# Optimization experiments

Hardware: AMD Instinct MI355X
Metric: run time of the kernel (lower is better)

The kernel has to match this reference:

```python
import jax, jax.numpy as jnp
import numpy as np

K = 20
EPS = 1e-5
SLOPE = 0.2


def _leaky(v):
    return jnp.where(v >= 0, v, SLOPE * v)


def _instnorm(v, axes):
    # InstanceNorm with affine=False: normalize per (batch, channel) over spatial axes,
    # biased variance, eps=1e-5 (torch default).
    mean = jnp.mean(v, axis=axes, keepdims=True)
    var = jnp.mean((v - mean) ** 2, axis=axes, keepdims=True)
    return (v - mean) * jax.lax.rsqrt(var + EPS)


def _knn_idx(x, k):
    # x: [B, C, N]; returns indices of k nearest neighbors (self included), [B, N, k]
    inner = -2.0 * jnp.einsum('bcn,bcm->bnm', x, x)
    xx = jnp.sum(x * x, axis=1)                      # [B, N]
    pd = -xx[:, :, None] - inner - xx[:, None, :]    # negative squared distance
    return jax.lax.top_k(pd, k)[1]


def _edge_conv(x, w):
    # x: [B, C, N]; w: [O, 2C]. Returns [B, O, N] after max-pool over k neighbors.
    B, C, N = x.shape
    idx = _knn_idx(x, K)                              # [B, N, K]
    xt = jnp.transpose(x, (0, 2, 1))                  # [B, N, C]
    b_idx = jnp.arange(B)[:, None, None]
    nb = xt[b_idx, idx]                               # [B, N, K, C] gathered neighbors
    ctr = xt[:, :, None, :]                           # [B, N, 1, C]
    feat = jnp.concatenate([nb - ctr, jnp.broadcast_to(ctr, nb.shape)], axis=-1)
    h = jnp.einsum('oc,bnkc->bonk', w, feat)          # 1x1 conv as GEMM -> [B, O, N, K]
    h = _leaky(_instnorm(h, (2, 3)))
    return jnp.max(h, axis=-1)                        # [B, O, N]


def setup_inputs() -> dict:
    key = jax.random.key(0)
    ks = jax.random.split(key, 6)
    B, N, feat_dim = 8, 2048, 512
    return {
        'x': jax.random.normal(ks[0], (B, N, 3), dtype=jnp.float32),
        'w1': jax.random.normal(ks[1], (64, 6), dtype=jnp.float32) * 0.1,
        'w2': jax.random.normal(ks[2], (64, 128), dtype=jnp.float32) * 0.1,
        'w3': jax.random.normal(ks[3], (128, 128), dtype=jnp.float32) * 0.1,
        'w4': jax.random.normal(ks[4], (256, 256), dtype=jnp.float32) * 0.1,
        'w5': jax.random.normal(ks[5], (feat_dim, 512), dtype=jnp.float32) * 0.1,
    }


def reference(x, w1, w2, w3, w4, w5):
    xc = jnp.transpose(x, (0, 2, 1))                  # [B, 3, N]
    x1 = _edge_conv(xc, w1)                           # [B, 64, N]
    x2 = _edge_conv(x1, w2)                           # [B, 64, N]
    x3 = _edge_conv(x2, w3)                           # [B, 128, N]
    x4 = _edge_conv(x3, w4)                           # [B, 256, N]
    cat = jnp.concatenate([x1, x2, x3, x4], axis=1)   # [B, 512, N]
    h = jnp.einsum('oc,bcn->bon', w5, cat)            # conv5 (1x1 conv1d)
    feat = _leaky(_instnorm(h, (2,)))
    return feat                                       # [B, feat_dim, N]
```

## Files before the change

kernel.cpp:

```cpp
#include <hip/hip_runtime.h>
#include <math.h>

#define NPTS 2048
#define NB 8
#define KNN 20
#define EPSI 1e-5f
#define SLOPE 0.2f
#define CHUNK 512

typedef short bf16x8 __attribute__((ext_vector_type(8)));
typedef float f32x4 __attribute__((ext_vector_type(4)));

__device__ __forceinline__ unsigned short f2bf(float x) {
    union { float f; unsigned u; } v; v.f = x;
    unsigned r = v.u + 0x7FFF + ((v.u >> 16) & 1u);
    return (unsigned short)(r >> 16);
}
__device__ __forceinline__ float bf2f(unsigned short h) {
    union { unsigned u; float f; } v; v.u = ((unsigned)h) << 16; return v.f;
}

__global__ __launch_bounds__(256) void transpose_kernel(const float* __restrict__ xin,
                                                        float* __restrict__ xc) {
    int g = blockIdx.x * 256 + threadIdx.x;
    int b = g / NPTS, n = g % NPTS;
    float v0 = xin[(size_t)g * 3 + 0];
    float v1 = xin[(size_t)g * 3 + 1];
    float v2 = xin[(size_t)g * 3 + 2];
    xc[((size_t)b * 3 + 0) * NPTS + n] = v0;
    xc[((size_t)b * 3 + 1) * NPTS + n] = v1;
    xc[((size_t)b * 3 + 2) * NPTS + n] = v2;
}

__global__ __launch_bounds__(256) void xx_kernel(const float* __restrict__ x, int bstride, int C,
                                                 float* __restrict__ xx) {
    int g = blockIdx.x * 256 + threadIdx.x;
    int b = g / NPTS, n = g % NPTS;
    const float* p = x + (size_t)b * bstride + n;
    float s = 0.f;
    for (int c = 0; c < C; ++c) { float v = p[(size_t)c * NPTS]; s += v * v; }
    xx[g] = s;
}

__global__ __launch_bounds__(256) void pd_gemm2(const float* __restrict__ x, int bstride, int C,
                                                const float* __restrict__ xx,
                                                float* __restrict__ pd, int r0) {
    __shared__ float As[16][128];
    __shared__ float Bs[16][128];
    int b = blockIdx.z;
    int nbase_l = blockIdx.y * 128;
    int mbase = blockIdx.x * 128;
    int tx = threadIdx.x & 15, ty = threadIdx.x >> 4;
    int tid = threadIdx.x;
    float acc[8][8] = {};
    const float* xb = x + (size_t)b * bstride;

    for (int c0 = 0; c0 < C; c0 += 16) {
        int KC = min(16, C - c0);
        for (int t = tid; t < 512; t += 256) {
            int cc = t >> 5, j4 = (t & 31) * 4;
            float4 av = make_float4(0.f, 0.f, 0.f, 0.f), bv = av;
            if (cc < KC) {
                av = *(const float4*)&xb[(size_t)(c0 + cc) * NPTS + r0 + nbase_l + j4];
                bv = *(const float4*)&xb[(size_t)(c0 + cc) * NPTS + mbase + j4];
            }
            *(float4*)&As[cc][j4] = av;
            *(float4*)&Bs[cc][j4] = bv;
        }
        __syncthreads();
        #pragma unroll
        for (int cc = 0; cc < 16; ++cc) {
            float av[8], bv[8];
            *(float4*)&av[0] = *(float4*)&As[cc][ty * 8];
            *(float4*)&av[4] = *(float4*)&As[cc][ty * 8 + 4];
            *(float4*)&bv[0] = *(float4*)&Bs[cc][tx * 8];
            *(float4*)&bv[4] = *(float4*)&Bs[cc][tx * 8 + 4];
            #pragma unroll
            for (int i = 0; i < 8; ++i)
                #pragma unroll
                for (int j = 0; j < 8; ++j)
                    acc[i][j] += av[i] * bv[j];
        }
        __syncthreads();
    }

    const float* xxb = xx + (size_t)b * NPTS;
    #pragma unroll
    for (int i = 0; i < 8; ++i) {
        int nl = nbase_l + ty * 8 + i;
        float xn = xxb[r0 + nl];
        float4 o0, o1;
        o0.x = 2.f * acc[i][0] - xn - xxb[mbase + tx*8 + 0];
        o0.y = 2.f * acc[i][1] - xn - xxb[mbase + tx*8 + 1];
        o0.z = 2.f * acc[i][2] - xn - xxb[mbase + tx*8 + 2];
        o0.w = 2.f * acc[i][3] - xn - xxb[mbase + tx*8 + 3];
        o1.x = 2.f * acc[i][4] - xn - xxb[mbase + tx*8 + 4];
        o1.y = 2.f * acc[i][5] - xn - xxb[mbase + tx*8 + 5];
        o1.z = 2.f * acc[i][6] - xn - xxb[mbase + tx*8 + 6];
        o1.w = 2.f * acc[i][7] - xn - xxb[mbase + tx*8 + 7];
        *(float4*)&pd[((size_t)b * CHUNK + nl) * NPTS + mbase + tx*8] = o0;
        *(float4*)&pd[((size_t)b * CHUNK + nl) * NPTS + mbase + tx*8 + 4] = o1;
    }
}

__global__ __launch_bounds__(256) void topk_kernel(const float* __restrict__ pd,
                                                   int* __restrict__ idxout, int r0) {
    int wid = (blockIdx.x * 256 + threadIdx.x) >> 6;
    int lane = threadIdx.x & 63;
    int b = wid / CHUNK;
    int nl = wid % CHUNK;
    int n = r0 + nl;
    const float* row = pd + ((size_t)b * CHUNK + nl) * NPTS;

    float v[32];
    #pragma unroll
    for (int j = 0; j < 32; ++j) v[j] = row[lane + 64 * j];

    unsigned mask = 0u;
    int saved = 0;
    for (int t = 0; t < KNN; ++t) {
        float best = -INFINITY; int bj = 0;
        #pragma unroll
        for (int j = 0; j < 32; ++j) {
            bool ok = ((mask >> j) & 1u) == 0u;
            if (ok && v[j] > best) { best = v[j]; bj = j; }
        }
        int midx = lane + 64 * bj;
        #pragma unroll
        for (int off = 32; off > 0; off >>= 1) {
            float ov = __shfl_xor(best, off);
            int om = __shfl_xor(midx, off);
            if (ov > best || (ov == best && om < midx)) { best = ov; midx = om; }
        }
        if (lane == t) saved = midx;
        if ((midx & 63) == lane) mask |= 1u << (midx >> 6);
    }
    if (lane < KNN) idxout[((size_t)b * NPTS + n) * KNN + lane] = saved;
}

__global__ __launch_bounds__(256) void yz_gemm(const float* __restrict__ x, int bstride, int C, int O,
                                               const float* __restrict__ w,
                                               float* __restrict__ y, float* __restrict__ z) {
    __shared__ float Xs[128 * 64];
    __shared__ float Ws[4 * 256];
    int b = blockIdx.z;
    int mbase = blockIdx.x * 64;
    int obase = blockIdx.y * 4;
    int tx = threadIdx.x & 63, ty = threadIdx.x >> 6;
    int tid = threadIdx.x;
    const float* xb = x + (size_t)b * bstride;

    for (int t = tid; t < C * 64; t += 256) {
        int cc = t >> 6, j = t & 63;
        Xs[cc * 64 + j] = xb[(size_t)cc * NPTS + mbase + j];
    }
    int C2 = 2 * C;
    for (int t = tid; t < 4 * C2; t += 256) {
        int ol = t / C2, c = t % C2;
        Ws[ol * C2 + c] = w[(size_t)(obase + ol) * C2 + c];
    }
    __syncthreads();

    int o = obase + ty;
    const float* wr = &Ws[ty * C2];
    float ya = 0.f, za = 0.f;
    for (int c = 0; c < C; ++c) {
        float v = Xs[c * 64 + tx];
        float wd = wr[c], wc = wr[C + c];
        ya += wd * v;
        za += (wc - wd) * v;
    }
    y[((size_t)b * O + o) * NPTS + mbase + tx] = ya;
    z[((size_t)b * O + o) * NPTS + mbase + tx] = za;
}

__global__ __launch_bounds__(256) void gather_norm(const float* __restrict__ y,
                                                   const float* __restrict__ z,
                                                   const int* __restrict__ idx,
                                                   float* __restrict__ cat, int coff, int O) {
    __shared__ float yrow[NPTS];
    __shared__ float red[8];
    int o = blockIdx.x, b = blockIdx.y;
    int tid = threadIdx.x;
    const float* yr = y + ((size_t)b * O + o) * NPTS;
    for (int i = tid; i < NPTS / 4; i += 256)
        ((float4*)yrow)[i] = ((const float4*)yr)[i];
    __syncthreads();

    const float* zr = z + ((size_t)b * O + o) * NPTS;
    float s1 = 0.f, s2 = 0.f;
    float hm[8];
    #pragma unroll
    for (int r = 0; r < 8; ++r) {
        int n = r * 256 + tid;
        float zv = zr[n];
        const int* ip = idx + ((size_t)b * NPTS + n) * KNN;
        float mx = -INFINITY;
        #pragma unroll
        for (int k = 0; k < KNN; ++k) {
            float h = yrow[ip[k]] + zv;
            s1 += h; s2 += h * h;
            mx = fmaxf(mx, h);
        }
        hm[r] = mx;
    }
    #pragma unroll
    for (int off = 32; off > 0; off >>= 1) {
        s1 += __shfl_xor(s1, off);
        s2 += __shfl_xor(s2, off);
    }
    int wv = tid >> 6, lane = tid & 63;
    if (lane == 0) { red[wv] = s1; red[4 + wv] = s2; }
    __syncthreads();
    float S1 = red[0] + red[1] + red[2] + red[3];
    float S2 = red[4] + red[5] + red[6] + red[7];
    const float inv = 1.f / (float)(NPTS * KNN);
    float mean = S1 * inv;
    float var = S2 * inv - mean * mean;
    float rs = 1.f / sqrtf(var + EPSI);
    float* dst = cat + ((size_t)b * 512 + coff + o) * NPTS;
    #pragma unroll
    for (int r = 0; r < 8; ++r) {
        float vv = (hm[r] - mean) * rs;
        dst[r * 256 + tid] = vv >= 0.f ? vv : SLOPE * vv;
    }
}

__global__ __launch_bounds__(256) void w5_prep(const float* __restrict__ w5,
                                               unsigned short* __restrict__ wh,
                                               unsigned short* __restrict__ wl) {
    int i = blockIdx.x * 256 + threadIdx.x;
    float x = w5[i];
    unsigned short h = f2bf(x);
    wh[i] = h;
    wl[i] = f2bf(x - bf2f(h));
}

__global__ __launch_bounds__(256) void catT_prep(const float* __restrict__ cat,
                                                 unsigned short* __restrict__ cth,
                                                 unsigned short* __restrict__ ctl) {
    __shared__ float t[32][33];
    int b = blockIdx.z;
    int n0 = blockIdx.x * 32, c0 = blockIdx.y * 32;
    int tx = threadIdx.x & 31, ty = threadIdx.x >> 5;
    #pragma unroll
    for (int r = 0; r < 4; ++r) {
        int ci = ty + r * 8;
        t[ci][tx] = cat[((size_t)b * 512 + c0 + ci) * NPTS + n0 + tx];
    }
    __syncthreads();
    #pragma unroll
    for (int r = 0; r < 4; ++r) {
        int ni = ty + r * 8;
        float x = t[tx][ni];
        unsigned short h = f2bf(x);
        size_t off = ((size_t)b * NPTS + n0 + ni) * 512 + c0 + tx;
        cth[off] = h;
        ctl[off] = f2bf(x - bf2f(h));
    }
}

__global__ __launch_bounds__(256) void final_gemm_mfma(const unsigned short* __restrict__ wh,
                                                       const unsigned short* __restrict__ wl,
                                                       const unsigned short* __restrict__ cth,
                                                       const unsigned short* __restrict__ ctl,
                                                       float* __restrict__ h) {
    int b = blockIdx.z;
    int nbase = blockIdx.x * 64, obase = blockIdx.y * 64;
    int w = threadIdx.x >> 6, l = threadIdx.x & 63;
    int wr = (w >> 1) * 32, wc = (w & 1) * 32;
    int lr = l & 15, lk = (l >> 4) * 8;

    f32x4 acc[2][2] = {};
    const unsigned short* aH = wh + (size_t)(obase + wr + lr) * 512 + lk;
    const unsigned short* aL = wl + (size_t)(obase + wr + lr) * 512 + lk;
    const unsigned short* bH = cth + ((size_t)b * NPTS + nbase + wc + lr) * 512 + lk;
    const unsigned short* bL = ctl + ((size_t)b * NPTS + nbase + wc + lr) * 512 + lk;

    for (int k0 = 0; k0 < 512; k0 += 32) {
        bf16x8 ah[2], al[2], bh[2], bl[2];
        #pragma unroll
        for (int mi = 0; mi < 2; ++mi) {
            ah[mi] = *(const bf16x8*)(aH + (size_t)mi * 16 * 512 + k0);
            al[mi] = *(const bf16x8*)(aL + (size_t)mi * 16 * 512 + k0);
        }
        #pragma unroll
        for (int ni = 0; ni < 2; ++ni) {
            bh[ni] = *(const bf16x8*)(bH + (size_t)ni * 16 * 512 + k0);
            bl[ni] = *(const bf16x8*)(bL + (size_t)ni * 16 * 512 + k0);
        }
        #pragma unroll
        for (int mi = 0; mi < 2; ++mi)
            #pragma unroll
            for (int ni = 0; ni < 2; ++ni) {
                acc[mi][ni] = __builtin_amdgcn_mfma_f32_16x16x32_bf16(ah[mi], bh[ni], acc[mi][ni], 0, 0, 0);
                acc[mi][ni] = __builtin_amdgcn_mfma_f32_16x16x32_bf16(ah[mi], bl[ni], acc[mi][ni], 0, 0, 0);
                acc[mi][ni] = __builtin_amdgcn_mfma_f32_16x16x32_bf16(al[mi], bh[ni], acc[mi][ni], 0, 0, 0);
            }
    }

    int orow = obase + wr + (l >> 4) * 4;
    int ncol = nbase + wc + lr;
    #pragma unroll
    for (int mi = 0; mi < 2; ++mi)
        #pragma unroll
        for (int r = 0; r < 4; ++r)
            #pragma unroll
            for (int ni = 0; ni < 2; ++ni)
                h[((size_t)b * 512 + orow + mi * 16 + r) * NPTS + ncol + ni * 16] = acc[mi][ni][r];
}

__global__ __launch_bounds__(256) void final_norm(const float* __restrict__ h,
                                                  float* __restrict__ out) {
    __shared__ float red[8];
    int o = blockIdx.x, b = blockIdx.y;
    int tid = threadIdx.x;
    const float* hr = h + ((size_t)b * 512 + o) * NPTS;
    float s1 = 0.f, s2 = 0.f;
    float v[8];
    #pragma unroll
    for (int r = 0; r < 8; ++r) {
        v[r] = hr[r * 256 + tid];
        s1 += v[r]; s2 += v[r] * v[r];
    }
    #pragma unroll
    for (int off = 32; off > 0; off >>= 1) {
        s1 += __shfl_xor(s1, off);
        s2 += __shfl_xor(s2, off);
    }
    int wv = tid >> 6, lane = tid & 63;
    if (lane == 0) { red[wv] = s1; red[4 + wv] = s2; }
    __syncthreads();
    float S1 = red[0] + red[1] + red[2] + red[3];
    float S2 = red[4] + red[5] + red[6] + red[7];
    const float inv = 1.f / (float)NPTS;
    float mean = S1 * inv;
    float var = S2 * inv - mean * mean;
    float rs = 1.f / sqrtf(var + EPSI);
    float* dst = out + ((size_t)b * 512 + o) * NPTS;
    #pragma unroll
    for (int r = 0; r < 8; ++r) {
        float vv = (v[r] - mean) * rs;
        dst[r * 256 + tid] = vv >= 0.f ? vv : SLOPE * vv;
    }
}

extern "C" void kernel_launch(void* const* d_in, const int* in_sizes, int n_in,
                              void* d_out, int out_size, void* d_ws, size_t ws_size,
                              hipStream_t stream) {
    const float* x_in = (const float*)d_in[0];
    const float* w1 = (const float*)d_in[1];
    const float* w2 = (const float*)d_in[2];
    const float* w3 = (const float*)d_in[3];
    const float* w4 = (const float*)d_in[4];
    const float* w5 = (const float*)d_in[5];
    float* out = (float*)d_out;
    float* ws = (float*)d_ws;

    float* region = ws;
    float* yb = region;
    float* zb = region + 4194304;
    float* pdb = region;
    int* idxb = (int*)(ws + 8388608);
    float* xxb = ws + 8388608 + 327680;
    float* xcb = xxb + NB * NPTS;
    float* cat = xcb + NB * 3 * NPTS;
    unsigned short* w5h = (unsigned short*)(cat + 8388608);
    unsigned short* w5l = w5h + 262144;
    unsigned short* cth = (unsigned short*)region;
    unsigned short* ctl = cth + (size_t)NB * NPTS * 512;
    float* hb = cat;

    transpose_kernel<<<NB * NPTS / 256, 256, 0, stream>>>(x_in, xcb);
    w5_prep<<<512 * 512 / 256, 256, 0, stream>>>(w5, w5h, w5l);

    const float* srcs[4] = {xcb, cat, cat + (size_t)64 * NPTS, cat + (size_t)128 * NPTS};
    int bstr[4] = {3 * NPTS, 512 * NPTS, 512 * NPTS, 512 * NPTS};
    int Cin[4] = {3, 64, 64, 128};
    int Oc[4] = {64, 64, 128, 256};
    const float* wl[4] = {w1, w2, w3, w4};
    int coffs[4] = {0, 64, 128, 256};

    for (int li = 0; li < 4; ++li) {
        xx_kernel<<<NB * NPTS / 256, 256, 0, stream>>>(srcs[li], bstr[li], Cin[li], xxb);
        for (int r0 = 0; r0 < NPTS; r0 += CHUNK) {
            pd_gemm2<<<dim3(NPTS / 128, CHUNK / 128, NB), 256, 0, stream>>>(
                srcs[li], bstr[li], Cin[li], xxb, pdb, r0);
            topk_kernel<<<NB * CHUNK / 4, 256, 0, stream>>>(pdb, idxb, r0);
        }
        yz_gemm<<<dim3(NPTS / 64, Oc[li] / 4, NB), dim3(256), 0, stream>>>(
            srcs[li], bstr[li], Cin[li], Oc[li], wl[li], yb, zb);
        gather_norm<<<dim3(Oc[li], NB), 256, 0, stream>>>(yb, zb, idxb, cat, coffs[li], Oc[li]);
    }

    catT_prep<<<dim3(NPTS / 32, 512 / 32, NB), 256, 0, stream>>>(cat, cth, ctl);
    final_gemm_mfma<<<dim3(NPTS / 64, 512 / 64, NB), 256, 0, stream>>>(w5h, w5l, cth, ctl, hb);
    final_norm<<<dim3(512, NB), 256, 0, stream>>>(hb, out);
}
```

Before: 1.530 ms.

## Double-buffer pd and final GEMMs, register-tile yz GEMM, batch channels in gather

The pairwise-distance GEMM now double-buffers its shared-memory tiles, so each iteration needs one barrier instead of two, and the final MFMA GEMM prefetches the next K-slice into registers. The yz GEMM is rewritten as a 64x64 register-tiled GEMM with K chunks staged in shared memory, replacing the one-output-per-thread dot product. gather_norm now handles four output channels per block, so each neighbour index load feeds four channels through a single float4 LDS read. The trade-off is higher register and LDS use, which may lower occupancy, and fewer blocks in the gather for small channel counts.

```diff
diff --git a/kernel.cpp b/kernel.cpp
--- a/kernel.cpp
+++ b/kernel.cpp
@@ -45,8 +45,8 @@
 __global__ __launch_bounds__(256) void pd_gemm2(const float* __restrict__ x, int bstride, int C,
                                                 const float* __restrict__ xx,
                                                 float* __restrict__ pd, int r0) {
-    __shared__ float As[16][128];
-    __shared__ float Bs[16][128];
+    __shared__ float As[2][16][128];
+    __shared__ float Bs[2][16][128];
     int b = blockIdx.z;
     int nbase_l = blockIdx.y * 128;
     int mbase = blockIdx.x * 128;
@@ -55,33 +55,68 @@
     float acc[8][8] = {};
     const float* xb = x + (size_t)b * bstride;
 
-    for (int c0 = 0; c0 < C; c0 += 16) {
-        int KC = min(16, C - c0);
+    {
+        int KC = min(16, C);
         for (int t = tid; t < 512; t += 256) {
             int cc = t >> 5, j4 = (t & 31) * 4;
             float4 av = make_float4(0.f, 0.f, 0.f, 0.f), bv = av;
             if (cc < KC) {
-                av = *(const float4*)&xb[(size_t)(c0 + cc) * NPTS + r0 + nbase_l + j4];
-                bv = *(const float4*)&xb[(size_t)(c0 + cc) * NPTS + mbase + j4];
-            }
-            *(float4*)&As[cc][j4] = av;
-            *(float4*)&Bs[cc][j4] = bv;
+                av = *(const float4*)&xb[(size_t)cc * NPTS + r0 + nbase_l + j4];
+                bv = *(const float4*)&xb[(size_t)cc * NPTS + mbase + j4];
+            }
+            *(float4*)&As[0][cc][j4] = av;
+            *(float4*)&Bs[0][cc][j4] = bv;
+        }
+    }
+    __syncthreads();
+
+    int cur = 0;
+    for (int c0 = 0; c0 < C; c0 += 16) {
+        int c1 = c0 + 16;
+        if (c1 < C) {
+            int KC = min(16, C - c1);
+            for (int t = tid; t < 512; t += 256) {
+                int cc = t >> 5, j4 = (t & 31) * 4;
+                float4 av = make_float4(0.f, 0.f, 0.f, 0.f), bv = av;
+                if (cc < KC) {
+                    av = *(const float4*)&xb[(size_t)(c1 + cc) * NPTS + r0 + nbase_l + j4];
+                    bv = *(const float4*)&xb[(size_t)(c1 + cc) * NPTS + mbase + j4];
+                }
+                *(float4*)&As[cur ^ 1][cc][j4] = av;
+                *(float4*)&Bs[cur ^ 1][cc][j4] = bv;
+            }
+        }
+        int KC = min(16, C - c0);
+        if (KC == 16) {
+            #pragma unroll
+            for (int cc = 0; cc < 16; ++cc) {
+                float av[8], bv[8];
+                *(float4*)&av[0] = *(float4*)&As[cur][cc][ty * 8];
+                *(float4*)&av[4] = *(float4*)&As[cur][cc][ty * 8 + 4];
+                *(float4*)&bv[0] = *(float4*)&Bs[cur][cc][tx * 8];
+                *(float4*)&bv[4] = *(float4*)&Bs[cur][cc][tx * 8 + 4];
+                #pragma unroll
+                for (int i = 0; i < 8; ++i)
+                    #pragma unroll
+                    for (int j = 0; j < 8; ++j)
+                        acc[i][j] += av[i] * bv[j];
+            }
+        } else {
+            for (int cc = 0; cc < KC; ++cc) {
+                float av[8], bv[8];
+                *(float4*)&av[0] = *(float4*)&As[cur][cc][ty * 8];
+                *(float4*)&av[4] = *(float4*)&As[cur][cc][ty * 8 + 4];
+                *(float4*)&bv[0] = *(float4*)&Bs[cur][cc][tx * 8];
+                *(float4*)&bv[4] = *(float4*)&Bs[cur][cc][tx * 8 + 4];
+                #pragma unroll
+                for (int i = 0; i < 8; ++i)
+                    #pragma unroll
+                    for (int j = 0; j < 8; ++j)
+                        acc[i][j] += av[i] * bv[j];
+            }
         }
         __syncthreads();
-        #pragma unroll
-        for (int cc = 0; cc < 16; ++cc) {
-            float av[8], bv[8];
-            *(float4*)&av[0] = *(float4*)&As[cc][ty * 8];
-            *(float4*)&av[4] = *(float4*)&As[cc][ty * 8 + 4];
-            *(float4*)&bv[0] = *(float4*)&Bs[cc][tx * 8];
-            *(float4*)&bv[4] = *(float4*)&Bs[cc][tx * 8 + 4];
-            #pragma unroll
-            for (int i = 0; i < 8; ++i)
-                #pragma unroll
-                for (int j = 0; j < 8; ++j)
-                    acc[i][j] += av[i] * bv[j];
-        }
-        __syncthreads();
+        cur ^= 1;
     }
 
     const float* xxb = xx + (size_t)b * NPTS;
@@ -138,91 +173,131 @@
     if (lane < KNN) idxout[((size_t)b * NPTS + n) * KNN + lane] = saved;
 }
 
-__global__ __launch_bounds__(256) void yz_gemm(const float* __restrict__ x, int bstride, int C, int O,
-                                               const float* __restrict__ w,
-                                               float* __restrict__ y, float* __restrict__ z) {
-    __shared__ float Xs[128 * 64];
-    __shared__ float Ws[4 * 256];
+__global__ __launch_bounds__(256) void yz_gemm2(const float* __restrict__ x, int bstride, int C, int O,
+                                                const float* __restrict__ w,
+                                                float* __restrict__ y, float* __restrict__ z) {
+    __shared__ float Xs[32][64];
+    __shared__ float Wd[32][64];
+    __shared__ float Wz[32][64];
     int b = blockIdx.z;
     int mbase = blockIdx.x * 64;
-    int obase = blockIdx.y * 4;
-    int tx = threadIdx.x & 63, ty = threadIdx.x >> 6;
+    int obase = blockIdx.y * 64;
     int tid = threadIdx.x;
+    int nq = tid & 15, oq = tid >> 4;
     const float* xb = x + (size_t)b * bstride;
-
-    for (int t = tid; t < C * 64; t += 256) {
-        int cc = t >> 6, j = t & 63;
-        Xs[cc * 64 + j] = xb[(size_t)cc * NPTS + mbase + j];
-    }
     int C2 = 2 * C;
-    for (int t = tid; t < 4 * C2; t += 256) {
-        int ol = t / C2, c = t % C2;
-        Ws[ol * C2 + c] = w[(size_t)(obase + ol) * C2 + c];
+    float accy[4][4] = {}, accz[4][4] = {};
+
+    for (int c0 = 0; c0 < C; c0 += 32) {
+        int KC = min(32, C - c0);
+        for (int t = tid; t < 512; t += 256) {
+            int cc = t >> 4, j4 = (t & 15) * 4;
+            float4 v = make_float4(0.f, 0.f, 0.f, 0.f);
+            if (cc < KC) v = *(const float4*)&xb[(size_t)(c0 + cc) * NPTS + mbase + j4];
+            *(float4*)&Xs[cc][j4] = v;
+        }
+        for (int t = tid; t < 2048; t += 256) {
+            int o = t >> 5, cc = t & 31;
+            float wd = 0.f, wz = 0.f;
+            if (cc < KC) {
+                wd = w[(size_t)(obase + o) * C2 + c0 + cc];
+                wz = w[(size_t)(obase + o) * C2 + C + c0 + cc] - wd;
+            }
+            Wd[cc][o] = wd; Wz[cc][o] = wz;
+        }
+        __syncthreads();
+        for (int cc = 0; cc < KC; ++cc) {
+            float xv[4], wdv[4], wzv[4];
+            *(float4*)xv  = *(float4*)&Xs[cc][nq * 4];
+            *(float4*)wdv = *(float4*)&Wd[cc][oq * 4];
+            *(float4*)wzv = *(float4*)&Wz[cc][oq * 4];
+            #pragma unroll
+            for (int i = 0; i < 4; ++i)
+                #pragma unroll
+                for (int j = 0; j < 4; ++j) {
+                    accy[i][j] += wdv[i] * xv[j];
+                    accz[i][j] += wzv[i] * xv[j];
+                }
+        }
+        __syncthreads();
+    }
+
+    #pragma unroll
+    for (int i = 0; i < 4; ++i) {
+        size_t off = ((size_t)b * O + obase + oq * 4 + i) * NPTS + mbase + nq * 4;
+        *(float4*)&y[off] = make_float4(accy[i][0], accy[i][1], accy[i][2], accy[i][3]);
+        *(float4*)&z[off] = make_float4(accz[i][0], accz[i][1], accz[i][2], accz[i][3]);
+    }
+}
+
+__global__ __launch_bounds__(256) void gather_norm2(const float* __restrict__ y,
+                                                    const float* __restrict__ z,
+                                                    const int* __restrict__ idx,
+                                                    float* __restrict__ cat, int coff, int O) {
+    __shared__ float yt[NPTS][4];
+    __shared__ float red[32];
+    int og = blockIdx.x * 4, b = blockIdx.y;
+    int tid = threadIdx.x;
+
+    for (int n = tid; n < NPTS; n += 256) {
+        float4 v;
+        v.x = y[((size_t)b * O + og + 0) * NPTS + n];
+        v.y = y[((size_t)b * O + og + 1) * NPTS + n];
+        v.z = y[((size_t)b * O + og + 2) * NPTS + n];
+        v.w = y[((size_t)b * O + og + 3) * NPTS + n];
+        *(float4*)&yt[n][0] = v;
     }
     __syncthreads();
 
-    int o = obase + ty;
-    const float* wr = &Ws[ty * C2];
-    float ya = 0.f, za = 0.f;
-    for (int c = 0; c < C; ++c) {
-        float v = Xs[c * 64 + tx];
-        float wd = wr[c], wc = wr[C + c];
-        ya += wd * v;
-        za += (wc - wd) * v;
-    }
-    y[((size_t)b * O + o) * NPTS + mbase + tx] = ya;
-    z[((size_t)b * O + o) * NPTS + mbase + tx] = za;
-}
-
-__global__ __launch_bounds__(256) void gather_norm(const float* __restrict__ y,
-                                                   const float* __restrict__ z,
-                                                   const int* __restrict__ idx,
-                                                   float* __restrict__ cat, int coff, int O) {
-    __shared__ float yrow[NPTS];
-    __shared__ float red[8];
-    int o = blockIdx.x, b = blockIdx.y;
-    int tid = threadIdx.x;
-    const float* yr = y + ((size_t)b * O + o) * NPTS;
-    for (int i = tid; i < NPTS / 4; i += 256)
-        ((float4*)yrow)[i] = ((const float4*)yr)[i];
-    __syncthreads();
-
-    const float* zr = z + ((size_t)b * O + o) * NPTS;
-    float s1 = 0.f, s2 = 0.f;
-    float hm[8];
-    #pragma unroll
+    float s1[4] = {0.f, 0.f, 0.f, 0.f}, s2[4] = {0.f, 0.f, 0.f, 0.f};
+    float hm[4][8];
     for (int r = 0; r < 8; ++r) {
         int n = r * 256 + tid;
-        float zv = zr[n];
         const int* ip = idx + ((size_t)b * NPTS + n) * KNN;
-        float mx = -INFINITY;
+        float zv[4], mx[4];
+        #pragma unroll
+        for (int j = 0; j < 4; ++j) {
+            zv[j] = z[((size_t)b * O + og + j) * NPTS + n];
+            mx[j] = -INFINITY;
+        }
         #pragma unroll
         for (int k = 0; k < KNN; ++k) {
-            float h = yrow[ip[k]] + zv;
-            s1 += h; s2 += h * h;
-            mx = fmaxf(mx, h);
-        }
-        hm[r] = mx;
-    }
-    #pragma unroll
-    for (int off = 32; off > 0; off >>= 1) {
-        s1 += __shfl_xor(s1, off);
-        s2 += __shfl_xor(s2, off);
-    }
+            int id = ip[k];
+            float4 yv = *(float4*)&yt[id][0];
+            float h0 = yv.x + zv[0]; s1[0] += h0; s2[0] += h0 * h0; mx[0] = fmaxf(mx[0], h0);
+            float h1 = yv.y + zv[1]; s1[1] += h1; s2[1] += h1 * h1; mx[1] = fmaxf(mx[1], h1);
+            float h2 = yv.z + zv[2]; s1[2] += h2; s2[2] += h2 * h2; mx[2] = fmaxf(mx[2], h2);
+            float h3 = yv.w + zv[3]; s1[3] += h3; s2[3] += h3 * h3; mx[3] = fmaxf(mx[3], h3);
+        }
+        #pragma unroll
+        for (int j = 0; j < 4; ++j) hm[j][r] = mx[j];
+    }
+    #pragma unroll
+    for (int off = 32; off > 0; off >>= 1)
+        #pragma unroll
+        for (int j = 0; j < 4; ++j) {
+            s1[j] += __shfl_xor(s1[j], off);
+            s2[j] += __shfl_xor(s2[j], off);
+        }
     int wv = tid >> 6, lane = tid & 63;
-    if (lane == 0) { red[wv] = s1; red[4 + wv] = s2; }
+    if (lane == 0)
+        #pragma unroll
+        for (int j = 0; j < 4; ++j) { red[j * 8 + wv] = s1[j]; red[j * 8 + 4 + wv] = s2[j]; }
     __syncthreads();
-    float S1 = red[0] + red[1] + red[2] + red[3];
-    float S2 = red[4] + red[5] + red[6] + red[7];
     const float inv = 1.f / (float)(NPTS * KNN);
-    float mean = S1 * inv;
-    float var = S2 * inv - mean * mean;
-    float rs = 1.f / sqrtf(var + EPSI);
-    float* dst = cat + ((size_t)b * 512 + coff + o) * NPTS;
-    #pragma unroll
-    for (int r = 0; r < 8; ++r) {
-        float vv = (hm[r] - mean) * rs;
-        dst[r * 256 + tid] = vv >= 0.f ? vv : SLOPE * vv;
+    #pragma unroll
+    for (int j = 0; j < 4; ++j) {
+        float S1 = red[j * 8 + 0] + red[j * 8 + 1] + red[j * 8 + 2] + red[j * 8 + 3];
+        float S2 = red[j * 8 + 4] + red[j * 8 + 5] + red[j * 8 + 6] + red[j * 8 + 7];
+        float mean = S1 * inv;
+        float var = S2 * inv - mean * mean;
+        float rs = 1.f / sqrtf(var + EPSI);
+        float* dst = cat + ((size_t)b * 512 + coff + og + j) * NPTS;
+        #pragma unroll
+        for (int r = 0; r < 8; ++r) {
+            float vv = (hm[j][r] - mean) * rs;
+            dst[r * 256 + tid] = vv >= 0.f ? vv : SLOPE * vv;
+        }
     }
 }
 
@@ -277,26 +352,36 @@
     const unsigned short* bH = cth + ((size_t)b * NPTS + nbase + wc + lr) * 512 + lk;
     const unsigned short* bL = ctl + ((size_t)b * NPTS + nbase + wc + lr) * 512 + lk;
 
+    bf16x8 ah[2][2], al[2][2], bh[2][2], bl[2][2];
+    #pragma unroll
+    for (int mi = 0; mi < 2; ++mi) {
+        ah[0][mi] = *(const bf16x8*)(aH + (size_t)mi * 16 * 512);
+        al[0][mi] = *(const bf16x8*)(aL + (size_t)mi * 16 * 512);
+        bh[0][mi] = *(const bf16x8*)(bH + (size_t)mi * 16 * 512);
+        bl[0][mi] = *(const bf16x8*)(bL + (size_t)mi * 16 * 512);
+    }
+
+    int buf = 0;
     for (int k0 = 0; k0 < 512; k0 += 32) {
-        bf16x8 ah[2], al[2], bh[2], bl[2];
-        #pragma unroll
-        for (int mi = 0; mi < 2; ++mi) {
-            ah[mi] = *(const bf16x8*)(aH + (size_t)mi * 16 * 512 + k0);
-            al[mi] = *(const bf16x8*)(aL + (size_t)mi * 16 * 512 + k0);
-        }
-        #pragma unroll
-        for (int ni = 0; ni < 2; ++ni) {
-            bh[ni] = *(const bf16x8*)(bH + (size_t)ni * 16 * 512 + k0);
-            bl[ni] = *(const bf16x8*)(bL + (size_t)ni * 16 * 512 + k0);
+        int nxt = buf ^ 1;
+        if (k0 + 32 < 512) {
+            #pragma unroll
+            for (int mi = 0; mi < 2; ++mi) {
+                ah[nxt][mi] = *(const bf16x8*)(aH + (size_t)mi * 16 * 512 + k0 + 32);
+                al[nxt][mi] = *(const bf16x8*)(aL + (size_t)mi * 16 * 512 + k0 + 32);
+                bh[nxt][mi] = *(const bf16x8*)(bH + (size_t)mi * 16 * 512 + k0 + 32);
+                bl[nxt][mi] = *(const bf16x8*)(bL + (size_t)mi * 16 * 512 + k0 + 32);
+            }
         }
         #pragma unroll
         for (int mi = 0; mi < 2; ++mi)
             #pragma unroll
             for (int ni = 0; ni < 2; ++ni) {
-                acc[mi][ni] = __builtin_amdgcn_mfma_f32_16x16x32_bf16(ah[mi], bh[ni], acc[mi][ni], 0, 0, 0);
-                acc[mi][ni] = __builtin_amdgcn_mfma_f32_16x16x32_bf16(ah[mi], bl[ni], acc[mi][ni], 0, 0, 0);
-                acc[mi][ni] = __builtin_amdgcn_mfma_f32_16x16x32_bf16(al[mi], bh[ni], acc[mi][ni], 0, 0, 0);
-            }
+                acc[mi][ni] = __builtin_amdgcn_mfma_f32_16x16x32_bf16(ah[buf][mi], bh[buf][ni], acc[mi][ni], 0, 0, 0);
+                acc[mi][ni] = __builtin_amdgcn_mfma_f32_16x16x32_bf16(ah[buf][mi], bl[buf][ni], acc[mi][ni], 0, 0, 0);
+                acc[mi][ni] = __builtin_amdgcn_mfma_f32_16x16x32_bf16(al[buf][mi], bh[buf][ni], acc[mi][ni], 0, 0, 0);
+            }
+        buf = nxt;
     }
 
     int orow = obase + wr + (l >> 4) * 4;
@@ -388,9 +473,9 @@
                 srcs[li], bstr[li], Cin[li], xxb, pdb, r0);
             topk_kernel<<<NB * CHUNK / 4, 256, 0, stream>>>(pdb, idxb, r0);
         }
-        yz_gemm<<<dim3(NPTS / 64, Oc[li] / 4, NB), dim3(256), 0, stream>>>(
+        yz_gemm2<<<dim3(NPTS / 64, Oc[li] / 64, NB), 256, 0, stream>>>(
             srcs[li], bstr[li], Cin[li], Oc[li], wl[li], yb, zb);
-        gather_norm<<<dim3(Oc[li], NB), 256, 0, stream>>>(yb, zb, idxb, cat, coffs[li], Oc[li]);
+        gather_norm2<<<dim3(Oc[li] / 4, NB), 256, 0, stream>>>(yb, zb, idxb, cat, coffs[li], Oc[li]);
     }
 
     catT_prep<<<dim3(NPTS / 32, 512 / 32, NB), 256, 0, stream>>>(cat, cth, ctl);
```

After: 1.448 ms. 5.4% less time.
